# Kernel tuning notes

Hardware: AMD Instinct MI355X
Metric: run time of the kernel (lower is better)

The kernel has to match this reference:

```python
import jax, jax.numpy as jnp
import numpy as np

N_MODELS = 128
N_FEAT = 32
TREE_LAYERS = [64, 32, 16]
INPUT_SIZE = 512
BATCH = 8192
EPS = 1e-5


def _uniform(key, shape, fan_in, fan_out):
    stdv = np.sqrt(6.0 / (fan_in + fan_out))
    return jax.random.uniform(key, shape, jnp.float32, -stdv, stdv)


def setup_inputs() -> dict:
    key = jax.random.key(0)
    ks = jax.random.split(key, 8)
    x = jax.random.normal(ks[0], (BATCH, INPUT_SIZE), jnp.float32)
    # flattened per-tree feature indices, shape [n_models * n_feature]
    used_features = jax.random.randint(ks[1], (N_MODELS * N_FEAT,), 0, INPUT_SIZE, jnp.int32)
    W1 = _uniform(ks[2], (N_MODELS, N_FEAT, TREE_LAYERS[0]), N_FEAT, TREE_LAYERS[0])
    b1 = jnp.zeros((N_MODELS, 1, TREE_LAYERS[0]), jnp.float32)
    W2 = _uniform(ks[3], (N_MODELS, TREE_LAYERS[0], TREE_LAYERS[1]), TREE_LAYERS[0], TREE_LAYERS[1])
    b2 = jnp.zeros((N_MODELS, 1, TREE_LAYERS[1]), jnp.float32)
    W3 = _uniform(ks[4], (N_MODELS, TREE_LAYERS[1], TREE_LAYERS[2]), TREE_LAYERS[1], TREE_LAYERS[2])
    b3 = jnp.zeros((N_MODELS, 1, TREE_LAYERS[2]), jnp.float32)
    gamma1 = jnp.ones((N_MODELS * TREE_LAYERS[0],), jnp.float32)
    beta1 = jnp.zeros((N_MODELS * TREE_LAYERS[0],), jnp.float32)
    gamma2 = jnp.ones((N_MODELS * TREE_LAYERS[1],), jnp.float32)
    beta2 = jnp.zeros((N_MODELS * TREE_LAYERS[1],), jnp.float32)
    out_weight = jax.random.normal(ks[5], (N_MODELS * TREE_LAYERS[2], 1), jnp.float32)
    out_bias = jnp.zeros((1,), jnp.float32)
    return {
        "x": x, "used_features": used_features,
        "W1": W1, "b1": b1, "W2": W2, "b2": b2, "W3": W3, "b3": b3,
        "gamma1": gamma1, "beta1": beta1, "gamma2": gamma2, "beta2": beta2,
        "out_weight": out_weight, "out_bias": out_bias,
    }


def _batch_dense(h, W, b):
    # h: [B, n_models, in], W: [n_models, in, out], b: [n_models, 1, out]
    return jnp.einsum("bmi,mio->bmo", h, W) + b[None, :, 0, :]


def _batchnorm_train(z, gamma, beta):
    # BatchNorm1d in training mode over 2D input: per-feature batch stats (biased var)
    mean = jnp.mean(z, axis=0)
    var = jnp.var(z, axis=0)
    return (z - mean) * jax.lax.rsqrt(var + EPS) * gamma + beta


def reference(x, used_features, W1, b1, W2, b2, W3, b3,
              gamma1, beta1, gamma2, beta2, out_weight, out_bias):
    B = x.shape[0]
    # gather used features: [B, n_models * n_feature] -> [B, n_models, n_feature]
    h = x[:, used_features].reshape(B, N_MODELS, N_FEAT)
    # layer 1: grouped GEMM + BN + ReLU
    h = _batch_dense(h, W1, b1).reshape(B, -1)
    h = jax.nn.relu(_batchnorm_train(h, gamma1, beta1))
    # layer 2
    h = _batch_dense(h.reshape(B, N_MODELS, -1), W2, b2).reshape(B, -1)
    h = jax.nn.relu(_batchnorm_train(h, gamma2, beta2))
    # last layer (no BN/ReLU) -> pred
    pred = _batch_dense(h.reshape(B, N_MODELS, -1), W3, b3).reshape(B, -1)
    out = pred @ out_weight + out_bias
    return (out, pred)
```

## Files before the change

kernel.cpp:

```cpp
#include <hip/hip_runtime.h>
#include <hip/hip_bf16.h>

#define BATCH   8192
#define NM      128
#define NF      32
#define L1      64
#define L2O     32
#define L3O     16
#define INSZ    512
#define EPSV    1e-5f
#define CH      16
#define P64     64
#define GS1B    256
#define XS_STR  522
#define H1STR   80
#define H2STR   40

typedef __attribute__((ext_vector_type(8))) short short8;
typedef __attribute__((ext_vector_type(4))) float f32x4;

union U8 { short8 s8; unsigned u[4]; };

__device__ inline unsigned short f2bf(float f) {
    union { float f; unsigned u; } v; v.f = f;
    return (unsigned short)((v.u + 0x7FFF + ((v.u >> 16) & 1)) >> 16);
}
__device__ inline unsigned pkbf(float a, float b) {
    union { __hip_bfloat162 h; unsigned u; } c;
    c.h = __float22bfloat162_rn(float2{a, b});
    return c.u;
}

__global__ __launch_bounds__(256) void k_prep(
    const float* __restrict__ W1, const float* __restrict__ W2,
    const float* __restrict__ W3,
    unsigned short* __restrict__ W1p, unsigned short* __restrict__ W2p,
    unsigned short* __restrict__ W3p)
{
    int g = blockIdx.x*256 + threadIdx.x;
    int m = g / 4608, r = g % 4608;
    if (r < 2048) {
        int n = r >> 9, l = (r >> 3) & 63, s = r & 7;
        W1p[m*2048 + r] = f2bf(W1[m*2048 + ((l>>4)*8+s)*L1 + n*16 + (l&15)]);
    } else if (r < 4096) {
        int q = r - 2048;
        int f = q >> 9, l = (q >> 3) & 63, s = q & 7;
        int n2 = f >> 1, ks = f & 1;
        W2p[m*2048 + q] = f2bf(W2[m*2048 + (ks*32+(l>>4)*8+s)*L2O + n2*16 + (l&15)]);
    } else {
        int q = r - 4096;
        int l = (q >> 3) & 63, s = q & 7;
        W3p[m*512 + q] = f2bf(W3[m*512 + ((l>>4)*8+s)*L3O + (l&15)]);
    }
}

__global__ __launch_bounds__(512) void k_gs1(
    const float* __restrict__ x, const int* __restrict__ uf,
    const unsigned short* __restrict__ W1p,
    unsigned short* __restrict__ Ag,
    float* __restrict__ s1sum, float* __restrict__ s1sq)
{
    __shared__ unsigned short xs[32*XS_STR];
    __shared__ int sUf[NM*NF];
    const int blk = blockIdx.x, t = threadIdx.x;
    #pragma unroll
    for (int p = 0; p < 8; ++p) {
        const float4 v = *(const float4*)(x + (size_t)blk*32*INSZ + p*2048 + t*4);
        const int row = 4*p + (t>>7), col = (t&127)*4;
        *(unsigned*)(&xs[row*XS_STR + col])     = pkbf(v.x, v.y);
        *(unsigned*)(&xs[row*XS_STR + col + 2]) = pkbf(v.z, v.w);
    }
    #pragma unroll
    for (int p = 0; p < 2; ++p)
        ((int4*)sUf)[t + p*512] = ((const int4*)uf)[t + p*512];
    __syncthreads();

    const int w = t >> 6, l = t & 63, lr = l & 15, lg = l >> 4;
    const unsigned short* xr0 = xs + lr*XS_STR;
    const unsigned short* xr1 = xs + (16+lr)*XS_STR;
    for (int mi = 0; mi < 16; ++mi) {
        const int m = w*16 + mi;
        const int4 ia = ((const int4*)sUf)[m*8 + lg*2];
        const int4 ib = ((const int4*)sUf)[m*8 + lg*2 + 1];
        U8 A0, A1;
        A0.u[0] = xr0[ia.x] | ((unsigned)xr0[ia.y] << 16);
        A0.u[1] = xr0[ia.z] | ((unsigned)xr0[ia.w] << 16);
        A0.u[2] = xr0[ib.x] | ((unsigned)xr0[ib.y] << 16);
        A0.u[3] = xr0[ib.z] | ((unsigned)xr0[ib.w] << 16);
        A1.u[0] = xr1[ia.x] | ((unsigned)xr1[ia.y] << 16);
        A1.u[1] = xr1[ia.z] | ((unsigned)xr1[ia.w] << 16);
        A1.u[2] = xr1[ib.x] | ((unsigned)xr1[ib.y] << 16);
        A1.u[3] = xr1[ib.z] | ((unsigned)xr1[ib.w] << 16);
        *(short8*)(Ag + ((size_t)(blk*2  )*NM + m)*512 + lr*32 + lg*8) = A0.s8;
        *(short8*)(Ag + ((size_t)(blk*2+1)*NM + m)*512 + lr*32 + lg*8) = A1.s8;
        float sum[4], sq[4];
        #pragma unroll
        for (int n = 0; n < 4; ++n) {
            const short8 wf = *(const short8*)(W1p + m*2048 + n*512 + l*8);
            f32x4 z = {0.f,0.f,0.f,0.f};
            f32x4 c0 = __builtin_amdgcn_mfma_f32_16x16x32_bf16(A0.s8, wf, z, 0, 0, 0);
            f32x4 c1 = __builtin_amdgcn_mfma_f32_16x16x32_bf16(A1.s8, wf, z, 0, 0, 0);
            sum[n] = (c0[0]+c0[1]) + (c0[2]+c0[3]) + (c1[0]+c1[1]) + (c1[2]+c1[3]);
            sq[n]  = c0[0]*c0[0] + c0[1]*c0[1] + c0[2]*c0[2] + c0[3]*c0[3]
                   + c1[0]*c1[0] + c1[1]*c1[1] + c1[2]*c1[2] + c1[3]*c1[3];
        }
        #pragma unroll
        for (int n = 0; n < 4; ++n) {
            sum[n] += __shfl_xor(sum[n], 16); sum[n] += __shfl_xor(sum[n], 32);
            sq[n]  += __shfl_xor(sq[n], 16);  sq[n]  += __shfl_xor(sq[n], 32);
        }
        if (l < 16) {
            #pragma unroll
            for (int n = 0; n < 4; ++n) {
                s1sum[(size_t)blk*8192 + m*64 + n*16 + l] = sum[n];
                s1sq [(size_t)blk*8192 + m*64 + n*16 + l] = sq[n];
            }
        }
    }
}

__global__ __launch_bounds__(256) void k_fin(
    const float* __restrict__ sump, const float* __restrict__ sqp,
    const float* __restrict__ bias, const float* __restrict__ gamma,
    const float* __restrict__ beta, float* __restrict__ scale,
    float* __restrict__ shift, int nfeat, int parts, int slotMajor)
{
    int f = blockIdx.x*256 + threadIdx.x;
    if (f >= nfeat) return;
    float S = 0.f, Q = 0.f;
    if (slotMajor) {
        #pragma unroll 8
        for (int c = 0; c < parts; ++c) { S += sump[(size_t)c*nfeat + f]; Q += sqp[(size_t)c*nfeat + f]; }
    } else {
        #pragma unroll 8
        for (int c = 0; c < parts; ++c) { S += sump[(size_t)f*parts + c]; Q += sqp[(size_t)f*parts + c]; }
    }
    float mz   = S * (1.f/BATCH);
    float var  = Q * (1.f/BATCH) - mz*mz;
    float mean = mz + bias[f];
    float sc   = rsqrtf(var + EPSV) * gamma[f];
    scale[f] = sc; shift[f] = beta[f] - mean*sc;
}

__global__ __launch_bounds__(256) void k_stats2_p(
    const unsigned short* __restrict__ Ag, const unsigned short* __restrict__ W1p,
    const float* __restrict__ scale1, const float* __restrict__ shift1,
    const unsigned short* __restrict__ W2p,
    float* __restrict__ sum2p, float* __restrict__ sq2p)
{
    __shared__ unsigned short h1T[4][16*H1STR];
    const int m = blockIdx.x >> 4, chunk = blockIdx.x & 15;
    const int t = threadIdx.x, w = t >> 6, l = t & 63;
    const int lr = l & 15, lg = l >> 4;
    short8 w1f[4];
    #pragma unroll
    for (int n = 0; n < 4; ++n) w1f[n] = *(const short8*)(W1p + m*2048 + n*512 + l*8);
    short8 w2f[2][2];
    #pragma unroll
    for (int n2 = 0; n2 < 2; ++n2)
        #pragma unroll
        for (int ks = 0; ks < 2; ++ks)
            w2f[n2][ks] = *(const short8*)(W2p + m*2048 + (n2*2+ks)*512 + l*8);
    float4 sc1q[4], sh1q[4];
    #pragma unroll
    for (int n = 0; n < 4; ++n) {
        sc1q[n] = *(const float4*)(scale1 + m*L1 + n*16 + lg*4);
        sh1q[n] = *(const float4*)(shift1 + m*L1 + n*16 + lg*4);
    }
    unsigned short* hT = &h1T[w][0];
    float sumf[8] = {0,0,0,0,0,0,0,0}, sqf[8] = {0,0,0,0,0,0,0,0};
    for (int i = 0; i < 8; ++i) {
        const int rbG = chunk*32 + i*4 + w;
        const short8 a = *(const short8*)(Ag + ((size_t)rbG*NM + m)*512 + lr*32 + lg*8);
        #pragma unroll
        for (int n = 0; n < 4; ++n) {
            f32x4 z = {0.f,0.f,0.f,0.f};
            f32x4 acc = __builtin_amdgcn_mfma_f32_16x16x32_bf16(w1f[n], a, z, 0, 0, 0);
            float h0 = acc[0]*sc1q[n].x + sh1q[n].x; h0 = h0 > 0.f ? h0 : 0.f;
            float h1 = acc[1]*sc1q[n].y + sh1q[n].y; h1 = h1 > 0.f ? h1 : 0.f;
            float h2 = acc[2]*sc1q[n].z + sh1q[n].z; h2 = h2 > 0.f ? h2 : 0.f;
            float h3 = acc[3]*sc1q[n].w + sh1q[n].w; h3 = h3 > 0.f ? h3 : 0.f;
            uint2 pk; pk.x = pkbf(h0, h1); pk.y = pkbf(h2, h3);
            *(uint2*)(hT + lr*H1STR + n*16 + lg*4) = pk;
        }
        const short8 a20 = *(const short8*)(hT + lr*H1STR + lg*8);
        const short8 a21 = *(const short8*)(hT + lr*H1STR + 32 + lg*8);
        #pragma unroll
        for (int n2 = 0; n2 < 2; ++n2) {
            f32x4 z = {0.f,0.f,0.f,0.f};
            f32x4 acc = __builtin_amdgcn_mfma_f32_16x16x32_bf16(w2f[n2][0], a20, z, 0, 0, 0);
            acc = __builtin_amdgcn_mfma_f32_16x16x32_bf16(w2f[n2][1], a21, acc, 0, 0, 0);
            #pragma unroll
            for (int r = 0; r < 4; ++r) {
                sumf[n2*4+r] += acc[r];
                sqf [n2*4+r] += acc[r]*acc[r];
            }
        }
    }
    #pragma unroll
    for (int j = 0; j < 8; ++j) {
        #pragma unroll
        for (int mk = 1; mk < 16; mk <<= 1) {
            sumf[j] += __shfl_xor(sumf[j], mk);
            sqf[j]  += __shfl_xor(sqf[j], mk);
        }
    }
    if (lr == 0) {
        const int slot = chunk*4 + w;
        #pragma unroll
        for (int n2 = 0; n2 < 2; ++n2)
            #pragma unroll
            for (int r = 0; r < 4; ++r) {
                const int f = m*L2O + n2*16 + lg*4 + r;
                sum2p[(size_t)f*P64 + slot] = sumf[n2*4+r];
                sq2p [(size_t)f*P64 + slot] = sqf[n2*4+r];
            }
    }
}

__global__ __launch_bounds__(256) void k_final_p(
    const unsigned short* __restrict__ Ag, const unsigned short* __restrict__ W1p,
    const float* __restrict__ scale1, const float* __restrict__ shift1,
    const unsigned short* __restrict__ W2p,
    const float* __restrict__ scale2, const float* __restrict__ shift2,
    const unsigned short* __restrict__ W3p, const float* __restrict__ b3,
    const float* __restrict__ ow,
    float* __restrict__ pred, float* __restrict__ outpartT)
{
    __shared__ unsigned short h1T[4][16*H1STR];
    __shared__ unsigned short h2T[4][16*H2STR];
    const int m = blockIdx.x >> 4, chunk = blockIdx.x & 15;
    const int t = threadIdx.x, w = t >> 6, l = t & 63;
    const int lr = l & 15, lg = l >> 4;
    short8 w1f[4];
    #pragma unroll
    for (int n = 0; n < 4; ++n) w1f[n] = *(const short8*)(W1p + m*2048 + n*512 + l*8);
    short8 w2f[2][2];
    #pragma unroll
    for (int n2 = 0; n2 < 2; ++n2)
        #pragma unroll
        for (int ks = 0; ks < 2; ++ks)
            w2f[n2][ks] = *(const short8*)(W2p + m*2048 + (n2*2+ks)*512 + l*8);
    const short8 w3f = *(const short8*)(W3p + m*512 + l*8);
    float4 sc1q[4], sh1q[4];
    #pragma unroll
    for (int n = 0; n < 4; ++n) {
        sc1q[n] = *(const float4*)(scale1 + m*L1 + n*16 + lg*4);
        sh1q[n] = *(const float4*)(shift1 + m*L1 + n*16 + lg*4);
    }
    float4 sc2q[2], sh2q[2];
    #pragma unroll
    for (int n2 = 0; n2 < 2; ++n2) {
        sc2q[n2] = *(const float4*)(scale2 + m*L2O + n2*16 + lg*4);
        sh2q[n2] = *(const float4*)(shift2 + m*L2O + n2*16 + lg*4);
    }
    const float4 b3f = *(const float4*)(b3 + m*L3O + lg*4);
    const float4 owf = *(const float4*)(ow + m*L3O + lg*4);
    unsigned short* hT  = &h1T[w][0];
    unsigned short* hT2 = &h2T[w][0];
    for (int i = 0; i < 8; ++i) {
        const int rbG = chunk*32 + i*4 + w;
        const short8 a = *(const short8*)(Ag + ((size_t)rbG*NM + m)*512 + lr*32 + lg*8);
        #pragma unroll
        for (int n = 0; n < 4; ++n) {
            f32x4 z = {0.f,0.f,0.f,0.f};
            f32x4 acc = __builtin_amdgcn_mfma_f32_16x16x32_bf16(w1f[n], a, z, 0, 0, 0);
            float h0 = acc[0]*sc1q[n].x + sh1q[n].x; h0 = h0 > 0.f ? h0 : 0.f;
            float h1 = acc[1]*sc1q[n].y + sh1q[n].y; h1 = h1 > 0.f ? h1 : 0.f;
            float h2 = acc[2]*sc1q[n].z + sh1q[n].z; h2 = h2 > 0.f ? h2 : 0.f;
            float h3 = acc[3]*sc1q[n].w + sh1q[n].w; h3 = h3 > 0.f ? h3 : 0.f;
            uint2 pk; pk.x = pkbf(h0, h1); pk.y = pkbf(h2, h3);
            *(uint2*)(hT + lr*H1STR + n*16 + lg*4) = pk;
        }
        const short8 a20 = *(const short8*)(hT + lr*H1STR + lg*8);
        const short8 a21 = *(const short8*)(hT + lr*H1STR + 32 + lg*8);
        #pragma unroll
        for (int n2 = 0; n2 < 2; ++n2) {
            f32x4 z = {0.f,0.f,0.f,0.f};
            f32x4 acc = __builtin_amdgcn_mfma_f32_16x16x32_bf16(w2f[n2][0], a20, z, 0, 0, 0);
            acc = __builtin_amdgcn_mfma_f32_16x16x32_bf16(w2f[n2][1], a21, acc, 0, 0, 0);
            float h0 = acc[0]*sc2q[n2].x + sh2q[n2].x; h0 = h0 > 0.f ? h0 : 0.f;
            float h1 = acc[1]*sc2q[n2].y + sh2q[n2].y; h1 = h1 > 0.f ? h1 : 0.f;
            float h2 = acc[2]*sc2q[n2].z + sh2q[n2].z; h2 = h2 > 0.f ? h2 : 0.f;
            float h3 = acc[3]*sc2q[n2].w + sh2q[n2].w; h3 = h3 > 0.f ? h3 : 0.f;
            uint2 pk; pk.x = pkbf(h0, h1); pk.y = pkbf(h2, h3);
            *(uint2*)(hT2 + lr*H2STR + n2*16 + lg*4) = pk;
        }
        {
            const short8 a3 = *(const short8*)(hT2 + lr*H2STR + lg*8);
            f32x4 z = {0.f,0.f,0.f,0.f};
            f32x4 acc = __builtin_amdgcn_mfma_f32_16x16x32_bf16(w3f, a3, z, 0, 0, 0);
            float4 pv;
            pv.x = acc[0] + b3f.x; pv.y = acc[1] + b3f.y;
            pv.z = acc[2] + b3f.z; pv.w = acc[3] + b3f.w;
            const size_t row = (size_t)rbG*16 + lr;
            *(float4*)(pred + row*(NM*L3O) + m*L3O + lg*4) = pv;
            float v = pv.x*owf.x + pv.y*owf.y + pv.z*owf.z + pv.w*owf.w;
            v += __shfl_xor(v, 16); v += __shfl_xor(v, 32);
            if (l < 16) outpartT[(size_t)m*BATCH + rbG*16 + l] = v;
        }
    }
}

__global__ __launch_bounds__(256) void k_outT(
    const float* __restrict__ outpartT, const float* __restrict__ ob,
    float* __restrict__ out)
{
    int b = blockIdx.x*256 + threadIdx.x;
    float acc = ob[0];
    #pragma unroll 8
    for (int m = 0; m < NM; ++m) acc += outpartT[(size_t)m*BATCH + b];
    out[b] = acc;
}

__global__ __launch_bounds__(256) void k_gather(
    const float* __restrict__ x, const int* __restrict__ uf,
    unsigned short* __restrict__ Ag)
{
    __shared__ float xs[16*INSZ];
    __shared__ int   sUf[NM*NF];
    const int rb = blockIdx.x;
    const int t  = threadIdx.x;
    const float4* xsrc = (const float4*)(x + (size_t)rb*16*INSZ);
    float4* xdst = (float4*)xs;
    #pragma unroll
    for (int p = 0; p < 8; ++p) xdst[t + p*256] = xsrc[t + p*256];
    const int4* us = (const int4*)uf;
    int4* ud = (int4*)sUf;
    #pragma unroll
    for (int p = 0; p < 4; ++p) ud[t + p*256] = us[t + p*256];
    __syncthreads();
    unsigned* outp = (unsigned*)(Ag + (size_t)rb*NM*512);
    const int e = t*2, r = e >> 5, j = e & 31;
    for (int m = 0; m < NM; ++m) {
        const int i0 = sUf[m*NF + j], i1 = sUf[m*NF + j + 1];
        outp[m*256 + t] = pkbf(xs[r*INSZ + i0], xs[r*INSZ + i1]);
    }
}

__global__ __launch_bounds__(256) void k_stats1_m(
    const unsigned short* __restrict__ Ag, const unsigned short* __restrict__ W1p,
    float* __restrict__ sum1p, float* __restrict__ sq1p)
{
    const int m = blockIdx.x >> 4, chunk = blockIdx.x & 15;
    const int t = threadIdx.x, w = t >> 6, l = t & 63;
    const int lr = l & 15, lg = l >> 4;
    short8 w1f[4];
    #pragma unroll
    for (int n = 0; n < 4; ++n) w1f[n] = *(const short8*)(W1p + m*2048 + n*512 + l*8);
    float sum[4] = {0,0,0,0}, sq[4] = {0,0,0,0};
    for (int i = 0; i < 8; ++i) {
        const int rbG = chunk*32 + i*4 + w;
        const short8 a = *(const short8*)(Ag + ((size_t)rbG*NM + m)*512 + lr*32 + lg*8);
        #pragma unroll
        for (int n = 0; n < 4; ++n) {
            f32x4 acc = {0.f,0.f,0.f,0.f};
            acc = __builtin_amdgcn_mfma_f32_16x16x32_bf16(a, w1f[n], acc, 0, 0, 0);
            sum[n] += (acc[0]+acc[1]) + (acc[2]+acc[3]);
            sq[n]  += acc[0]*acc[0] + acc[1]*acc[1] + acc[2]*acc[2] + acc[3]*acc[3];
        }
    }
    #pragma unroll
    for (int n = 0; n < 4; ++n) {
        sum[n] += __shfl_xor(sum[n], 16); sum[n] += __shfl_xor(sum[n], 32);
        sq[n]  += __shfl_xor(sq[n], 16);  sq[n]  += __shfl_xor(sq[n], 32);
    }
    if (l < 16) {
        const int slot = chunk*4 + w;
        #pragma unroll
        for (int n = 0; n < 4; ++n) {
            const int f = m*L1 + n*16 + l;
            sum1p[(size_t)f*P64 + slot] = sum[n];
            sq1p [(size_t)f*P64 + slot] = sq[n];
        }
    }
}

extern "C" void kernel_launch(void* const* d_in, const int* in_sizes, int n_in,
                              void* d_out, int out_size, void* d_ws, size_t ws_size,
                              hipStream_t stream) {
    const float* x   = (const float*)d_in[0];
    const int*   uf  = (const int*  )d_in[1];
    const float* W1  = (const float*)d_in[2];
    const float* b1  = (const float*)d_in[3];
    const float* W2  = (const float*)d_in[4];
    const float* b2  = (const float*)d_in[5];
    const float* W3  = (const float*)d_in[6];
    const float* b3  = (const float*)d_in[7];
    const float* g1  = (const float*)d_in[8];
    const float* be1 = (const float*)d_in[9];
    const float* g2  = (const float*)d_in[10];
    const float* be2 = (const float*)d_in[11];
    const float* ow  = (const float*)d_in[12];
    const float* ob  = (const float*)d_in[13];

    float* out  = (float*)d_out;
    float* pred = out + BATCH;

    const size_t agElems = (size_t)BATCH * NM * NF;
    unsigned short* Ag  = (unsigned short*)d_ws;
    unsigned short* W1p = Ag + agElems;
    unsigned short* W2p = W1p + NM*2048;
    unsigned short* W3p = W2p + NM*2048;
    float* scale1 = (float*)(W3p + NM*512);
    float* shift1 = scale1 + NM*L1;
    float* scale2 = shift1 + NM*L1;
    float* shift2 = scale2 + NM*L2O;
    float* arena  = shift2 + NM*L2O;
    const size_t prefixBytes = (char*)arena - (char*)d_ws;

    const size_t arenaA = (size_t)GS1B*8192*4*2;
    const size_t s2Bytes = (size_t)NM*L2O*P64*4*2;
    const size_t needA = prefixBytes + arenaA;
    const size_t arenaB = (size_t)NM*L1*P64*4*2;
    (void)s2Bytes;

    k_prep<<<NM*4608/256, 256, 0, stream>>>(W1, W2, W3, W1p, W2p, W3p);

    if (ws_size >= needA) {
        float* s1sum = arena;
        float* s1sq  = s1sum + (size_t)GS1B*8192;
        float* s2sum = arena;
        float* s2sq  = s2sum + (size_t)NM*L2O*P64;
        float* outpartT = arena;

        k_gs1<<<GS1B, 512, 0, stream>>>(x, uf, W1p, Ag, s1sum, s1sq);
        k_fin<<<NM*L1/256, 256, 0, stream>>>(s1sum, s1sq, b1, g1, be1, scale1, shift1, NM*L1, GS1B, 1);
        k_stats2_p<<<NM*CH, 256, 0, stream>>>(Ag, W1p, scale1, shift1, W2p, s2sum, s2sq);
        k_fin<<<NM*L2O/256, 256, 0, stream>>>(s2sum, s2sq, b2, g2, be2, scale2, shift2, NM*L2O, P64, 0);
        k_final_p<<<NM*CH, 256, 0, stream>>>(Ag, W1p, scale1, shift1, W2p, scale2, shift2,
                                             W3p, b3, ow, pred, outpartT);
        k_outT<<<BATCH/256, 256, 0, stream>>>(outpartT, ob, out);
    } else {
        float* s1sum = arena;
        float* s1sq  = s1sum + (size_t)NM*L1*P64;
        float* outpartT = arena;
        float* s2sum = arena + arenaB/4;
        float* s2sq  = s2sum + (size_t)NM*L2O*P64;

        k_gather<<<BATCH/16, 256, 0, stream>>>(x, uf, Ag);
        k_stats1_m<<<NM*CH, 256, 0, stream>>>(Ag, W1p, s1sum, s1sq);
        k_fin<<<NM*L1/256, 256, 0, stream>>>(s1sum, s1sq, b1, g1, be1, scale1, shift1, NM*L1, P64, 0);
        k_stats2_p<<<NM*CH, 256, 0, stream>>>(Ag, W1p, scale1, shift1, W2p, s2sum, s2sq);
        k_fin<<<NM*L2O/256, 256, 0, stream>>>(s2sum, s2sq, b2, g2, be2, scale2, shift2, NM*L2O, P64, 0);
        k_final_p<<<NM*CH, 256, 0, stream>>>(Ag, W1p, scale1, shift1, W2p, scale2, shift2,
                                             W3p, b3, ow, pred, outpartT);
        k_outT<<<BATCH/256, 256, 0, stream>>>(outpartT, ob, out);
    }
}
```

Before: 115.4 us.

## Fuse whole MLP pipeline into one cooperative persistent kernel with grid syncs

Replaces the chain of gather, stats, finalize and output kernels with a single cooperative kernel of 256 blocks. Each block keeps its 32 input rows in LDS and regathers features for every phase, separated by grid-wide syncs for the BatchNorm statistics. This removes the global gathered-activation buffer, the per-tree output partials and the extra reduction kernel, so there are fewer launches and less memory traffic. In exchange each block recomputes layer 1 three times and layer 2 twice, with only 256 blocks of 8 waves resident. It needs cooperative launch support and falls back to the multi-kernel path when that launch fails.

```diff
diff --git a/kernel.cpp b/kernel.cpp
--- a/kernel.cpp
+++ b/kernel.cpp
@@ -1,5 +1,8 @@
 #include <hip/hip_runtime.h>
 #include <hip/hip_bf16.h>
+#include <hip/hip_cooperative_groups.h>
+
+namespace cg = cooperative_groups;
 
 #define BATCH   8192
 #define NM      128
@@ -54,6 +57,295 @@
     }
 }
 
+__device__ __forceinline__ void gatherAB(
+    const unsigned short* xr0, const unsigned short* xr1,
+    const int* sUf, int m, int lg, U8& A0, U8& A1)
+{
+    const int4 ia = ((const int4*)sUf)[m*8 + lg*2];
+    const int4 ib = ((const int4*)sUf)[m*8 + lg*2 + 1];
+    A0.u[0] = xr0[ia.x] | ((unsigned)xr0[ia.y] << 16);
+    A0.u[1] = xr0[ia.z] | ((unsigned)xr0[ia.w] << 16);
+    A0.u[2] = xr0[ib.x] | ((unsigned)xr0[ib.y] << 16);
+    A0.u[3] = xr0[ib.z] | ((unsigned)xr0[ib.w] << 16);
+    A1.u[0] = xr1[ia.x] | ((unsigned)xr1[ia.y] << 16);
+    A1.u[1] = xr1[ia.z] | ((unsigned)xr1[ia.w] << 16);
+    A1.u[2] = xr1[ib.x] | ((unsigned)xr1[ib.y] << 16);
+    A1.u[3] = xr1[ib.z] | ((unsigned)xr1[ib.w] << 16);
+}
+
+__device__ __forceinline__ void d1_tile(
+    const short8 a, const short8* w1f,
+    const float4* sc1q, const float4* sh1q,
+    unsigned short* hT, int lr, int lg)
+{
+    #pragma unroll
+    for (int n = 0; n < 4; ++n) {
+        f32x4 z = {0.f,0.f,0.f,0.f};
+        f32x4 acc = __builtin_amdgcn_mfma_f32_16x16x32_bf16(w1f[n], a, z, 0, 0, 0);
+        float h0 = acc[0]*sc1q[n].x + sh1q[n].x; h0 = h0 > 0.f ? h0 : 0.f;
+        float h1 = acc[1]*sc1q[n].y + sh1q[n].y; h1 = h1 > 0.f ? h1 : 0.f;
+        float h2 = acc[2]*sc1q[n].z + sh1q[n].z; h2 = h2 > 0.f ? h2 : 0.f;
+        float h3 = acc[3]*sc1q[n].w + sh1q[n].w; h3 = h3 > 0.f ? h3 : 0.f;
+        uint2 pk; pk.x = pkbf(h0, h1); pk.y = pkbf(h2, h3);
+        *(uint2*)(hT + lr*H1STR + n*16 + lg*4) = pk;
+    }
+}
+
+__device__ __forceinline__ float fin_tile_v(
+    const unsigned short* hT, unsigned short* hT2,
+    const short8 (*w2f)[2], const short8 w3f,
+    const float4* sc2q, const float4* sh2q,
+    const float4 b3f, const float4 owf,
+    int lr, int lg, int m, int rbG, float* __restrict__ pred)
+{
+    const short8 a20 = *(const short8*)(hT + lr*H1STR + lg*8);
+    const short8 a21 = *(const short8*)(hT + lr*H1STR + 32 + lg*8);
+    #pragma unroll
+    for (int n2 = 0; n2 < 2; ++n2) {
+        f32x4 z = {0.f,0.f,0.f,0.f};
+        f32x4 acc = __builtin_amdgcn_mfma_f32_16x16x32_bf16(w2f[n2][0], a20, z, 0, 0, 0);
+        acc = __builtin_amdgcn_mfma_f32_16x16x32_bf16(w2f[n2][1], a21, acc, 0, 0, 0);
+        float h0 = acc[0]*sc2q[n2].x + sh2q[n2].x; h0 = h0 > 0.f ? h0 : 0.f;
+        float h1 = acc[1]*sc2q[n2].y + sh2q[n2].y; h1 = h1 > 0.f ? h1 : 0.f;
+        float h2 = acc[2]*sc2q[n2].z + sh2q[n2].z; h2 = h2 > 0.f ? h2 : 0.f;
+        float h3 = acc[3]*sc2q[n2].w + sh2q[n2].w; h3 = h3 > 0.f ? h3 : 0.f;
+        uint2 pk; pk.x = pkbf(h0, h1); pk.y = pkbf(h2, h3);
+        *(uint2*)(hT2 + lr*H2STR + n2*16 + lg*4) = pk;
+    }
+    const short8 a3 = *(const short8*)(hT2 + lr*H2STR + lg*8);
+    f32x4 z = {0.f,0.f,0.f,0.f};
+    f32x4 acc = __builtin_amdgcn_mfma_f32_16x16x32_bf16(w3f, a3, z, 0, 0, 0);
+    float4 pv;
+    pv.x = acc[0] + b3f.x; pv.y = acc[1] + b3f.y;
+    pv.z = acc[2] + b3f.z; pv.w = acc[3] + b3f.w;
+    const size_t row = (size_t)rbG*16 + lr;
+    *(float4*)(pred + row*(NM*L3O) + m*L3O + lg*4) = pv;
+    float v = pv.x*owf.x + pv.y*owf.y + pv.z*owf.z + pv.w*owf.w;
+    v += __shfl_xor(v, 16); v += __shfl_xor(v, 32);
+    return v;
+}
+
+struct MegaArgs {
+    const float* x; const int* uf;
+    const unsigned short *W1p, *W2p, *W3p;
+    const float *b1, *g1, *be1, *b2, *g2, *be2, *b3, *ow, *ob;
+    float *scale1, *shift1, *scale2, *shift2;
+    float *s1sum, *s1sq, *s2sum, *s2sq;
+    float *pred, *out;
+};
+
+__global__ __launch_bounds__(512, 2) void k_mega(MegaArgs A)
+{
+    cg::grid_group gg = cg::this_grid();
+    __shared__ unsigned short xs[32*XS_STR];
+    __shared__ int sUf[NM*NF];
+    __shared__ unsigned short h1A[8][16*H1STR];
+    __shared__ unsigned short h1B[8][16*H1STR];
+    __shared__ unsigned short h2A[8][16*H2STR];
+    __shared__ unsigned short h2B[8][16*H2STR];
+    __shared__ float outLds[8][32];
+
+    const int blk = blockIdx.x, t = threadIdx.x;
+    #pragma unroll
+    for (int p = 0; p < 8; ++p) {
+        const float4 v = *(const float4*)(A.x + (size_t)blk*32*INSZ + p*2048 + t*4);
+        const int row = 4*p + (t>>7), col = (t&127)*4;
+        *(unsigned*)(&xs[row*XS_STR + col])     = pkbf(v.x, v.y);
+        *(unsigned*)(&xs[row*XS_STR + col + 2]) = pkbf(v.z, v.w);
+    }
+    #pragma unroll
+    for (int p = 0; p < 2; ++p)
+        ((int4*)sUf)[t + p*512] = ((const int4*)A.uf)[t + p*512];
+    __syncthreads();
+
+    const int w = t >> 6, l = t & 63, lr = l & 15, lg = l >> 4;
+    const unsigned short* xr0 = xs + lr*XS_STR;
+    const unsigned short* xr1 = xs + (16+lr)*XS_STR;
+
+    for (int mi = 0; mi < 16; ++mi) {
+        const int m = w*16 + mi;
+        U8 A0, A1;
+        gatherAB(xr0, xr1, sUf, m, lg, A0, A1);
+        float sum[4], sq[4];
+        #pragma unroll
+        for (int n = 0; n < 4; ++n) {
+            const short8 wf = *(const short8*)(A.W1p + m*2048 + n*512 + l*8);
+            f32x4 z = {0.f,0.f,0.f,0.f};
+            f32x4 c0 = __builtin_amdgcn_mfma_f32_16x16x32_bf16(A0.s8, wf, z, 0, 0, 0);
+            f32x4 c1 = __builtin_amdgcn_mfma_f32_16x16x32_bf16(A1.s8, wf, z, 0, 0, 0);
+            sum[n] = (c0[0]+c0[1]) + (c0[2]+c0[3]) + (c1[0]+c1[1]) + (c1[2]+c1[3]);
+            sq[n]  = c0[0]*c0[0] + c0[1]*c0[1] + c0[2]*c0[2] + c0[3]*c0[3]
+                   + c1[0]*c1[0] + c1[1]*c1[1] + c1[2]*c1[2] + c1[3]*c1[3];
+        }
+        #pragma unroll
+        for (int n = 0; n < 4; ++n) {
+            sum[n] += __shfl_xor(sum[n], 16); sum[n] += __shfl_xor(sum[n], 32);
+            sq[n]  += __shfl_xor(sq[n], 16);  sq[n]  += __shfl_xor(sq[n], 32);
+        }
+        if (l < 16) {
+            #pragma unroll
+            for (int n = 0; n < 4; ++n) {
+                A.s1sum[(size_t)blk*8192 + m*64 + n*16 + l] = sum[n];
+                A.s1sq [(size_t)blk*8192 + m*64 + n*16 + l] = sq[n];
+            }
+        }
+    }
+    __threadfence();
+    gg.sync();
+
+    {
+        const int fl = t >> 4, slice = t & 15;
+        const int f = blk*32 + fl;
+        float S = 0.f, Q = 0.f;
+        #pragma unroll 4
+        for (int k = 0; k < 16; ++k) {
+            const int c = slice + k*16;
+            S += A.s1sum[(size_t)c*8192 + f];
+            Q += A.s1sq [(size_t)c*8192 + f];
+        }
+        #pragma unroll
+        for (int mk = 1; mk < 16; mk <<= 1) { S += __shfl_xor(S, mk); Q += __shfl_xor(Q, mk); }
+        if (slice == 0) {
+            float mz   = S * (1.f/BATCH);
+            float var  = Q * (1.f/BATCH) - mz*mz;
+            float mean = mz + A.b1[f];
+            float sc   = rsqrtf(var + EPSV) * A.g1[f];
+            A.scale1[f] = sc; A.shift1[f] = A.be1[f] - mean*sc;
+        }
+    }
+    __threadfence();
+    gg.sync();
+
+    for (int mi = 0; mi < 16; ++mi) {
+        const int m = w*16 + mi;
+        U8 A0, A1;
+        gatherAB(xr0, xr1, sUf, m, lg, A0, A1);
+        short8 w1f[4];
+        #pragma unroll
+        for (int n = 0; n < 4; ++n) w1f[n] = *(const short8*)(A.W1p + m*2048 + n*512 + l*8);
+        float4 sc1q[4], sh1q[4];
+        #pragma unroll
+        for (int n = 0; n < 4; ++n) {
+            sc1q[n] = *(const float4*)(A.scale1 + m*L1 + n*16 + lg*4);
+            sh1q[n] = *(const float4*)(A.shift1 + m*L1 + n*16 + lg*4);
+        }
+        unsigned short* hTa = &h1A[w][0];
+        unsigned short* hTb = &h1B[w][0];
+        d1_tile(A0.s8, w1f, sc1q, sh1q, hTa, lr, lg);
+        d1_tile(A1.s8, w1f, sc1q, sh1q, hTb, lr, lg);
+        short8 w2f[2][2];
+        #pragma unroll
+        for (int n2 = 0; n2 < 2; ++n2)
+            #pragma unroll
+            for (int ks = 0; ks < 2; ++ks)
+                w2f[n2][ks] = *(const short8*)(A.W2p + m*2048 + (n2*2+ks)*512 + l*8);
+        float sumf[8] = {0,0,0,0,0,0,0,0}, sqf[8] = {0,0,0,0,0,0,0,0};
+        #pragma unroll
+        for (int half = 0; half < 2; ++half) {
+            const unsigned short* hT = half ? hTb : hTa;
+            const short8 a20 = *(const short8*)(hT + lr*H1STR + lg*8);
+            const short8 a21 = *(const short8*)(hT + lr*H1STR + 32 + lg*8);
+            #pragma unroll
+            for (int n2 = 0; n2 < 2; ++n2) {
+                f32x4 z = {0.f,0.f,0.f,0.f};
+                f32x4 acc = __builtin_amdgcn_mfma_f32_16x16x32_bf16(w2f[n2][0], a20, z, 0, 0, 0);
+                acc = __builtin_amdgcn_mfma_f32_16x16x32_bf16(w2f[n2][1], a21, acc, 0, 0, 0);
+                #pragma unroll
+                for (int r = 0; r < 4; ++r) { sumf[n2*4+r] += acc[r]; sqf[n2*4+r] += acc[r]*acc[r]; }
+            }
+        }
+        #pragma unroll
+        for (int j = 0; j < 8; ++j) {
+            #pragma unroll
+            for (int mk = 1; mk < 16; mk <<= 1) {
+                sumf[j] += __shfl_xor(sumf[j], mk);
+                sqf[j]  += __shfl_xor(sqf[j], mk);
+            }
+        }
+        if (lr == 0) {
+            #pragma unroll
+            for (int n2 = 0; n2 < 2; ++n2)
+                #pragma unroll
+                for (int r = 0; r < 4; ++r) {
+                    const int f = m*L2O + n2*16 + lg*4 + r;
+                    A.s2sum[(size_t)blk*4096 + f] = sumf[n2*4+r];
+                    A.s2sq [(size_t)blk*4096 + f] = sqf[n2*4+r];
+                }
+        }
+    }
+    __threadfence();
+    gg.sync();
+
+    {
+        const int fl = t >> 5, slice = t & 31;
+        const int f = blk*16 + fl;
+        float S = 0.f, Q = 0.f;
+        #pragma unroll
+        for (int k = 0; k < 8; ++k) {
+            const int c = slice + k*32;
+            S += A.s2sum[(size_t)c*4096 + f];
+            Q += A.s2sq [(size_t)c*4096 + f];
+        }
+        #pragma unroll
+        for (int mk = 1; mk < 32; mk <<= 1) { S += __shfl_xor(S, mk); Q += __shfl_xor(Q, mk); }
+        if (slice == 0) {
+            float mz   = S * (1.f/BATCH);
+            float var  = Q * (1.f/BATCH) - mz*mz;
+            float mean = mz + A.b2[f];
+            float sc   = rsqrtf(var + EPSV) * A.g2[f];
+            A.scale2[f] = sc; A.shift2[f] = A.be2[f] - mean*sc;
+        }
+    }
+    __threadfence();
+    gg.sync();
+
+    float vacc0 = 0.f, vacc1 = 0.f;
+    const int rbG0 = blk*2, rbG1 = blk*2 + 1;
+    for (int mi = 0; mi < 16; ++mi) {
+        const int m = w*16 + mi;
+        U8 A0, A1;
+        gatherAB(xr0, xr1, sUf, m, lg, A0, A1);
+        short8 w1f[4];
+        #pragma unroll
+        for (int n = 0; n < 4; ++n) w1f[n] = *(const short8*)(A.W1p + m*2048 + n*512 + l*8);
+        float4 sc1q[4], sh1q[4];
+        #pragma unroll
+        for (int n = 0; n < 4; ++n) {
+            sc1q[n] = *(const float4*)(A.scale1 + m*L1 + n*16 + lg*4);
+            sh1q[n] = *(const float4*)(A.shift1 + m*L1 + n*16 + lg*4);
+        }
+        unsigned short* hTa = &h1A[w][0];
+        unsigned short* hTb = &h1B[w][0];
+        d1_tile(A0.s8, w1f, sc1q, sh1q, hTa, lr, lg);
+        d1_tile(A1.s8, w1f, sc1q, sh1q, hTb, lr, lg);
+        short8 w2f[2][2];
+        #pragma unroll
+        for (int n2 = 0; n2 < 2; ++n2)
+            #pragma unroll
+            for (int ks = 0; ks < 2; ++ks)
+                w2f[n2][ks] = *(const short8*)(A.W2p + m*2048 + (n2*2+ks)*512 + l*8);
+        float4 sc2q[2], sh2q[2];
+        #pragma unroll
+        for (int n2 = 0; n2 < 2; ++n2) {
+            sc2q[n2] = *(const float4*)(A.scale2 + m*L2O + n2*16 + lg*4);
+            sh2q[n2] = *(const float4*)(A.shift2 + m*L2O + n2*16 + lg*4);
+        }
+        const short8 w3f = *(const short8*)(A.W3p + m*512 + l*8);
+        const float4 b3f = *(const float4*)(A.b3 + m*L3O + lg*4);
+        const float4 owf = *(const float4*)(A.ow + m*L3O + lg*4);
+        vacc0 += fin_tile_v(hTa, &h2A[w][0], w2f, w3f, sc2q, sh2q, b3f, owf, lr, lg, m, rbG0, A.pred);
+        vacc1 += fin_tile_v(hTb, &h2B[w][0], w2f, w3f, sc2q, sh2q, b3f, owf, lr, lg, m, rbG1, A.pred);
+    }
+    if (l < 16) { outLds[w][lr] = vacc0; outLds[w][16 + lr] = vacc1; }
+    __syncthreads();
+    if (t < 32) {
+        float s = A.ob[0];
+        #pragma unroll
+        for (int w2 = 0; w2 < 8; ++w2) s += outLds[w2][t];
+        A.out[blk*32 + t] = s;
+    }
+}
+
 __global__ __launch_bounds__(512) void k_gs1(
     const float* __restrict__ x, const int* __restrict__ uf,
     const unsigned short* __restrict__ W1p,
@@ -74,23 +366,13 @@
     for (int p = 0; p < 2; ++p)
         ((int4*)sUf)[t + p*512] = ((const int4*)uf)[t + p*512];
     __syncthreads();
-
     const int w = t >> 6, l = t & 63, lr = l & 15, lg = l >> 4;
     const unsigned short* xr0 = xs + lr*XS_STR;
     const unsigned short* xr1 = xs + (16+lr)*XS_STR;
     for (int mi = 0; mi < 16; ++mi) {
         const int m = w*16 + mi;
-        const int4 ia = ((const int4*)sUf)[m*8 + lg*2];
-        const int4 ib = ((const int4*)sUf)[m*8 + lg*2 + 1];
         U8 A0, A1;
-        A0.u[0] = xr0[ia.x] | ((unsigned)xr0[ia.y] << 16);
-        A0.u[1] = xr0[ia.z] | ((unsigned)xr0[ia.w] << 16);
-        A0.u[2] = xr0[ib.x] | ((unsigned)xr0[ib.y] << 16);
-        A0.u[3] = xr0[ib.z] | ((unsigned)xr0[ib.w] << 16);
-        A1.u[0] = xr1[ia.x] | ((unsigned)xr1[ia.y] << 16);
-        A1.u[1] = xr1[ia.z] | ((unsigned)xr1[ia.w] << 16);
-        A1.u[2] = xr1[ib.x] | ((unsigned)xr1[ib.y] << 16);
-        A1.u[3] = xr1[ib.z] | ((unsigned)xr1[ib.w] << 16);
+        gatherAB(xr0, xr1, sUf, m, lg, A0, A1);
         *(short8*)(Ag + ((size_t)(blk*2  )*NM + m)*512 + lr*32 + lg*8) = A0.s8;
         *(short8*)(Ag + ((size_t)(blk*2+1)*NM + m)*512 + lr*32 + lg*8) = A1.s8;
         float sum[4], sq[4];
@@ -172,17 +454,7 @@
     for (int i = 0; i < 8; ++i) {
         const int rbG = chunk*32 + i*4 + w;
         const short8 a = *(const short8*)(Ag + ((size_t)rbG*NM + m)*512 + lr*32 + lg*8);
-        #pragma unroll
-        for (int n = 0; n < 4; ++n) {
-            f32x4 z = {0.f,0.f,0.f,0.f};
-            f32x4 acc = __builtin_amdgcn_mfma_f32_16x16x32_bf16(w1f[n], a, z, 0, 0, 0);
-            float h0 = acc[0]*sc1q[n].x + sh1q[n].x; h0 = h0 > 0.f ? h0 : 0.f;
-            float h1 = acc[1]*sc1q[n].y + sh1q[n].y; h1 = h1 > 0.f ? h1 : 0.f;
-            float h2 = acc[2]*sc1q[n].z + sh1q[n].z; h2 = h2 > 0.f ? h2 : 0.f;
-            float h3 = acc[3]*sc1q[n].w + sh1q[n].w; h3 = h3 > 0.f ? h3 : 0.f;
-            uint2 pk; pk.x = pkbf(h0, h1); pk.y = pkbf(h2, h3);
-            *(uint2*)(hT + lr*H1STR + n*16 + lg*4) = pk;
-        }
+        d1_tile(a, w1f, sc1q, sh1q, hT, lr, lg);
         const short8 a20 = *(const short8*)(hT + lr*H1STR + lg*8);
         const short8 a21 = *(const short8*)(hT + lr*H1STR + 32 + lg*8);
         #pragma unroll
@@ -191,10 +463,7 @@
             f32x4 acc = __builtin_amdgcn_mfma_f32_16x16x32_bf16(w2f[n2][0], a20, z, 0, 0, 0);
             acc = __builtin_amdgcn_mfma_f32_16x16x32_bf16(w2f[n2][1], a21, acc, 0, 0, 0);
             #pragma unroll
-            for (int r = 0; r < 4; ++r) {
-                sumf[n2*4+r] += acc[r];
-                sqf [n2*4+r] += acc[r]*acc[r];
-            }
+            for (int r = 0; r < 4; ++r) { sumf[n2*4+r] += acc[r]; sqf[n2*4+r] += acc[r]*acc[r]; }
         }
     }
     #pragma unroll
@@ -261,44 +530,9 @@
     for (int i = 0; i < 8; ++i) {
         const int rbG = chunk*32 + i*4 + w;
         const short8 a = *(const short8*)(Ag + ((size_t)rbG*NM + m)*512 + lr*32 + lg*8);
-        #pragma unroll
-        for (int n = 0; n < 4; ++n) {
-            f32x4 z = {0.f,0.f,0.f,0.f};
-            f32x4 acc = __builtin_amdgcn_mfma_f32_16x16x32_bf16(w1f[n], a, z, 0, 0, 0);
-            float h0 = acc[0]*sc1q[n].x + sh1q[n].x; h0 = h0 > 0.f ? h0 : 0.f;
-            float h1 = acc[1]*sc1q[n].y + sh1q[n].y; h1 = h1 > 0.f ? h1 : 0.f;
-            float h2 = acc[2]*sc1q[n].z + sh1q[n].z; h2 = h2 > 0.f ? h2 : 0.f;
-            float h3 = acc[3]*sc1q[n].w + sh1q[n].w; h3 = h3 > 0.f ? h3 : 0.f;
-            uint2 pk; pk.x = pkbf(h0, h1); pk.y = pkbf(h2, h3);
-            *(uint2*)(hT + lr*H1STR + n*16 + lg*4) = pk;
-        }
-        const short8 a20 = *(const short8*)(hT + lr*H1STR + lg*8);
-        const short8 a21 = *(const short8*)(hT + lr*H1STR + 32 + lg*8);
-        #pragma unroll
-        for (int n2 = 0; n2 < 2; ++n2) {
-            f32x4 z = {0.f,0.f,0.f,0.f};
-            f32x4 acc = __builtin_amdgcn_mfma_f32_16x16x32_bf16(w2f[n2][0], a20, z, 0, 0, 0);
-            acc = __builtin_amdgcn_mfma_f32_16x16x32_bf16(w2f[n2][1], a21, acc, 0, 0, 0);
-            float h0 = acc[0]*sc2q[n2].x + sh2q[n2].x; h0 = h0 > 0.f ? h0 : 0.f;
-            float h1 = acc[1]*sc2q[n2].y + sh2q[n2].y; h1 = h1 > 0.f ? h1 : 0.f;
-            float h2 = acc[2]*sc2q[n2].z + sh2q[n2].z; h2 = h2 > 0.f ? h2 : 0.f;
-            float h3 = acc[3]*sc2q[n2].w + sh2q[n2].w; h3 = h3 > 0.f ? h3 : 0.f;
-            uint2 pk; pk.x = pkbf(h0, h1); pk.y = pkbf(h2, h3);
-            *(uint2*)(hT2 + lr*H2STR + n2*16 + lg*4) = pk;
-        }
-        {
-            const short8 a3 = *(const short8*)(hT2 + lr*H2STR + lg*8);
-            f32x4 z = {0.f,0.f,0.f,0.f};
-            f32x4 acc = __builtin_amdgcn_mfma_f32_16x16x32_bf16(w3f, a3, z, 0, 0, 0);
-            float4 pv;
-            pv.x = acc[0] + b3f.x; pv.y = acc[1] + b3f.y;
-            pv.z = acc[2] + b3f.z; pv.w = acc[3] + b3f.w;
-            const size_t row = (size_t)rbG*16 + lr;
-            *(float4*)(pred + row*(NM*L3O) + m*L3O + lg*4) = pv;
-            float v = pv.x*owf.x + pv.y*owf.y + pv.z*owf.z + pv.w*owf.w;
-            v += __shfl_xor(v, 16); v += __shfl_xor(v, 32);
-            if (l < 16) outpartT[(size_t)m*BATCH + rbG*16 + l] = v;
-        }
+        d1_tile(a, w1f, sc1q, sh1q, hT, lr, lg);
+        float v = fin_tile_v(hT, hT2, w2f, w3f, sc2q, sh2q, b3f, owf, lr, lg, m, rbG, pred);
+        if (l < 16) outpartT[(size_t)m*BATCH + rbG*16 + l] = v;
     }
 }
 
@@ -311,69 +545,6 @@
     #pragma unroll 8
     for (int m = 0; m < NM; ++m) acc += outpartT[(size_t)m*BATCH + b];
     out[b] = acc;
-}
-
-__global__ __launch_bounds__(256) void k_gather(
-    const float* __restrict__ x, const int* __restrict__ uf,
-    unsigned short* __restrict__ Ag)
-{
-    __shared__ float xs[16*INSZ];
-    __shared__ int   sUf[NM*NF];
-    const int rb = blockIdx.x;
-    const int t  = threadIdx.x;
-    const float4* xsrc = (const float4*)(x + (size_t)rb*16*INSZ);
-    float4* xdst = (float4*)xs;
-    #pragma unroll
-    for (int p = 0; p < 8; ++p) xdst[t + p*256] = xsrc[t + p*256];
-    const int4* us = (const int4*)uf;
-    int4* ud = (int4*)sUf;
-    #pragma unroll
-    for (int p = 0; p < 4; ++p) ud[t + p*256] = us[t + p*256];
-    __syncthreads();
-    unsigned* outp = (unsigned*)(Ag + (size_t)rb*NM*512);
-    const int e = t*2, r = e >> 5, j = e & 31;
-    for (int m = 0; m < NM; ++m) {
-        const int i0 = sUf[m*NF + j], i1 = sUf[m*NF + j + 1];
-        outp[m*256 + t] = pkbf(xs[r*INSZ + i0], xs[r*INSZ + i1]);
-    }
-}
-
-__global__ __launch_bounds__(256) void k_stats1_m(
-    const unsigned short* __restrict__ Ag, const unsigned short* __restrict__ W1p,
-    float* __restrict__ sum1p, float* __restrict__ sq1p)
-{
-    const int m = blockIdx.x >> 4, chunk = blockIdx.x & 15;
-    const int t = threadIdx.x, w = t >> 6, l = t & 63;
-    const int lr = l & 15, lg = l >> 4;
-    short8 w1f[4];
-    #pragma unroll
-    for (int n = 0; n < 4; ++n) w1f[n] = *(const short8*)(W1p + m*2048 + n*512 + l*8);
-    float sum[4] = {0,0,0,0}, sq[4] = {0,0,0,0};
-    for (int i = 0; i < 8; ++i) {
-        const int rbG = chunk*32 + i*4 + w;
-        const short8 a = *(const short8*)(Ag + ((size_t)rbG*NM + m)*512 + lr*32 + lg*8);
-        #pragma unroll
-        for (int n = 0; n < 4; ++n) {
-            f32x4 acc = {0.f,0.f,0.f,0.f};
-            acc = __builtin_amdgcn_mfma_f32_16x16x32_bf16(a, w1f[n], acc, 0, 0, 0);
-            sum[n] += (acc[0]+acc[1]) + (acc[2]+acc[3]);
-            sq[n]  += acc[0]*acc[0] + acc[1]*acc[1] + acc[2]*acc[2] + acc[3]*acc[3];
-        }
-    }
-    #pragma unroll
-    for (int n = 0; n < 4; ++n) {
-        sum[n] += __shfl_xor(sum[n], 16); sum[n] += __shfl_xor(sum[n], 32);
-        sq[n]  += __shfl_xor(sq[n], 16);  sq[n]  += __shfl_xor(sq[n], 32);
-    }
-    if (l < 16) {
-        const int slot = chunk*4 + w;
-        #pragma unroll
-        for (int n = 0; n < 4; ++n) {
-            const int f = m*L1 + n*16 + l;
-            sum1p[(size_t)f*P64 + slot] = sum[n];
-            sq1p [(size_t)f*P64 + slot] = sq[n];
-        }
-    }
 }
 
 extern "C" void kernel_launch(void* const* d_in, const int* in_sizes, int n_in,
@@ -397,54 +568,58 @@
     float* out  = (float*)d_out;
     float* pred = out + BATCH;
 
-    const size_t agElems = (size_t)BATCH * NM * NF;
-    unsigned short* Ag  = (unsigned short*)d_ws;
-    unsigned short* W1p = Ag + agElems;
+    unsigned short* W1p = (unsigned short*)d_ws;
     unsigned short* W2p = W1p + NM*2048;
     unsigned short* W3p = W2p + NM*2048;
     float* scale1 = (float*)(W3p + NM*512);
     float* shift1 = scale1 + NM*L1;
     float* scale2 = shift1 + NM*L1;
     float* shift2 = scale2 + NM*L2O;
-    float* arena  = shift2 + NM*L2O;
-    const size_t prefixBytes = (char*)arena - (char*)d_ws;
-
-    const size_t arenaA = (size_t)GS1B*8192*4*2;
-    const size_t s2Bytes = (size_t)NM*L2O*P64*4*2;
-    const size_t needA = prefixBytes + arenaA;
-    const size_t arenaB = (size_t)NM*L1*P64*4*2;
-    (void)s2Bytes;
+    float* s1sum  = shift2 + NM*L2O;
+    float* s1sq   = s1sum + (size_t)GS1B*8192;
+    float* s2sum  = s1sq  + (size_t)GS1B*8192;
+    float* s2sq   = s2sum + (size_t)GS1B*4096;
+    float* after  = s2sq  + (size_t)GS1B*4096;
+    const size_t megaBytes = (char*)after - (char*)d_ws;
 
     k_prep<<<NM*4608/256, 256, 0, stream>>>(W1, W2, W3, W1p, W2p, W3p);
 
-    if (ws_size >= needA) {
-        float* s1sum = arena;
-        float* s1sq  = s1sum + (size_t)GS1B*8192;
-        float* s2sum = arena;
-        float* s2sq  = s2sum + (size_t)NM*L2O*P64;
-        float* outpartT = arena;
+    int dev = 0, coop = 0;
+    hipGetDevice(&dev);
+    hipDeviceGetAttribute(&coop, hipDeviceAttributeCooperativeLaunch, dev);
+
+    bool launched = false;
+    if (coop && ws_size >= megaBytes) {
+        MegaArgs margs;
+        margs.x = x; margs.uf = uf;
+        margs.W1p = W1p; margs.W2p = W2p; margs.W3p = W3p;
+        margs.b1 = b1; margs.g1 = g1; margs.be1 = be1;
+        margs.b2 = b2; margs.g2 = g2; margs.be2 = be2;
+        margs.b3 = b3; margs.ow = ow; margs.ob = ob;
+        margs.scale1 = scale1; margs.shift1 = shift1;
+        margs.scale2 = scale2; margs.shift2 = shift2;
+        margs.s1sum = s1sum; margs.s1sq = s1sq;
+        margs.s2sum = s2sum; margs.s2sq = s2sq;
+        margs.pred = pred; margs.out = out;
+        void* params[] = { &margs };
+        hipError_t e = hipLaunchCooperativeKernel((const void*)k_mega,
+                                                  dim3(GS1B), dim3(512), params, 0, stream);
+        launched = (e == hipSuccess);
+    }
+
+    if (!launched) {
+        unsigned short* Ag = (unsigned short*)after;
+        float* arena = (float*)(Ag + (size_t)BATCH*NM*NF);
+        float* f_s2sum = arena;
+        float* f_s2sq  = f_s2sum + (size_t)NM*L2O*P64;
+        float* outpartT = f_s2sq + (size_t)NM*L2O*P64;
 
         k_gs1<<<GS1B, 512, 0, stream>>>(x, uf, W1p, Ag, s1sum, s1sq);
         k_fin<<<NM*L1/256, 256, 0, stream>>>(s1sum, s1sq, b1, g1, be1, scale1, shift1, NM*L1, GS1B, 1);
-        k_stats2_p<<<NM*CH, 256, 0, stream>>>(Ag, W1p, scale1, shift1, W2p, s2sum, s2sq);
-        k_fin<<<NM*L2O/256, 256, 0, stream>>>(s2sum, s2sq, b2, g2, be2, scale2, shift2, NM*L2O, P64, 0);
+        k_stats2_p<<<NM*CH, 256, 0, stream>>>(Ag, W1p, scale1, shift1, W2p, f_s2sum, f_s2sq);
+        k_fin<<<NM*L2O/256, 256, 0, stream>>>(f_s2sum, f_s2sq, b2, g2, be2, scale2, shift2, NM*L2O, P64, 0);
         k_final_p<<<NM*CH, 256, 0, stream>>>(Ag, W1p, scale1, shift1, W2p, scale2, shift2,
                                              W3p, b3, ow, pred, outpartT);
         k_outT<<<BATCH/256, 256, 0, stream>>>(outpartT, ob, out);
-    } else {
-        float* s1sum = arena;
-        float* s1sq  = s1sum + (size_t)NM*L1*P64;
-        float* outpartT = arena;
-        float* s2sum = arena + arenaB/4;
-        float* s2sq  = s2sum + (size_t)NM*L2O*P64;
-
-        k_gather<<<BATCH/16, 256, 0, stream>>>(x, uf, Ag);
-        k_stats1_m<<<NM*CH, 256, 0, stream>>>(Ag, W1p, s1sum, s1sq);
-        k_fin<<<NM*L1/256, 256, 0, stream>>>(s1sum, s1sq, b1, g1, be1, scale1, shift1, NM*L1, P64, 0);
-        k_stats2_p<<<NM*CH, 256, 0, stream>>>(Ag, W1p, scale1, shift1, W2p, s2sum, s2sq);
-        k_fin<<<NM*L2O/256, 256, 0, stream>>>(s2sum, s2sq, b2, g2, be2, scale2, shift2, NM*L2O, P64, 0);
-        k_final_p<<<NM*CH, 256, 0, stream>>>(Ag, W1p, scale1, shift1, W2p, scale2, shift2,
-                                             W3p, b3, ow, pred, outpartT);
-        k_outT<<<BATCH/256, 256, 0, stream>>>(outpartT, ob, out);
-    }
-}
+    }
+}
```

Result: slower. 424.0 us (+267.3%).

## Halve rows per k_gs1 block, drop LDS index staging, fold b3 into MFMA

Applied to the files above, without the earlier changes.

The gather+stats1 kernel now uses 512 blocks of 16 rows each instead of 256 blocks of 32 rows. That halves shared memory per block, removes the used_features staging into LDS (indices are read from global/cache instead), and is meant to raise occupancy and grid coverage on the CUs. The price is twice as many per-block partial stat rows for k_fin to reduce and a larger workspace arena, which could push execution onto the fallback path if the workspace is too small. Separately, the final kernel passes the b3 bias as the MFMA accumulator input instead of adding it afterward.

```diff
diff --git a/kernel.cpp b/kernel.cpp
--- a/kernel.cpp
+++ b/kernel.cpp
@@ -11,7 +11,7 @@
 #define EPSV    1e-5f
 #define CH      16
 #define P64     64
-#define GS1B    256
+#define GS1B    512
 #define XS_STR  522
 #define H1STR   80
 #define H2STR   40
@@ -60,49 +60,37 @@
     unsigned short* __restrict__ Ag,
     float* __restrict__ s1sum, float* __restrict__ s1sq)
 {
-    __shared__ unsigned short xs[32*XS_STR];
-    __shared__ int sUf[NM*NF];
+    __shared__ unsigned short xs[16*XS_STR];
     const int blk = blockIdx.x, t = threadIdx.x;
     #pragma unroll
-    for (int p = 0; p < 8; ++p) {
-        const float4 v = *(const float4*)(x + (size_t)blk*32*INSZ + p*2048 + t*4);
+    for (int p = 0; p < 4; ++p) {
+        const float4 v = *(const float4*)(x + (size_t)blk*16*INSZ + p*2048 + t*4);
         const int row = 4*p + (t>>7), col = (t&127)*4;
         *(unsigned*)(&xs[row*XS_STR + col])     = pkbf(v.x, v.y);
         *(unsigned*)(&xs[row*XS_STR + col + 2]) = pkbf(v.z, v.w);
     }
-    #pragma unroll
-    for (int p = 0; p < 2; ++p)
-        ((int4*)sUf)[t + p*512] = ((const int4*)uf)[t + p*512];
     __syncthreads();
 
     const int w = t >> 6, l = t & 63, lr = l & 15, lg = l >> 4;
     const unsigned short* xr0 = xs + lr*XS_STR;
-    const unsigned short* xr1 = xs + (16+lr)*XS_STR;
     for (int mi = 0; mi < 16; ++mi) {
         const int m = w*16 + mi;
-        const int4 ia = ((const int4*)sUf)[m*8 + lg*2];
-        const int4 ib = ((const int4*)sUf)[m*8 + lg*2 + 1];
-        U8 A0, A1;
+        const int4 ia = ((const int4*)uf)[m*8 + lg*2];
+        const int4 ib = ((const int4*)uf)[m*8 + lg*2 + 1];
+        U8 A0;
         A0.u[0] = xr0[ia.x] | ((unsigned)xr0[ia.y] << 16);
         A0.u[1] = xr0[ia.z] | ((unsigned)xr0[ia.w] << 16);
         A0.u[2] = xr0[ib.x] | ((unsigned)xr0[ib.y] << 16);
         A0.u[3] = xr0[ib.z] | ((unsigned)xr0[ib.w] << 16);
-        A1.u[0] = xr1[ia.x] | ((unsigned)xr1[ia.y] << 16);
-        A1.u[1] = xr1[ia.z] | ((unsigned)xr1[ia.w] << 16);
-        A1.u[2] = xr1[ib.x] | ((unsigned)xr1[ib.y] << 16);
-        A1.u[3] = xr1[ib.z] | ((unsigned)xr1[ib.w] << 16);
-        *(short8*)(Ag + ((size_t)(blk*2  )*NM + m)*512 + lr*32 + lg*8) = A0.s8;
-        *(short8*)(Ag + ((size_t)(blk*2+1)*NM + m)*512 + lr*32 + lg*8) = A1.s8;
+        *(short8*)(Ag + ((size_t)blk*NM + m)*512 + lr*32 + lg*8) = A0.s8;
         float sum[4], sq[4];
         #pragma unroll
         for (int n = 0; n < 4; ++n) {
             const short8 wf = *(const short8*)(W1p + m*2048 + n*512 + l*8);
             f32x4 z = {0.f,0.f,0.f,0.f};
             f32x4 c0 = __builtin_amdgcn_mfma_f32_16x16x32_bf16(A0.s8, wf, z, 0, 0, 0);
-            f32x4 c1 = __builtin_amdgcn_mfma_f32_16x16x32_bf16(A1.s8, wf, z, 0, 0, 0);
-            sum[n] = (c0[0]+c0[1]) + (c0[2]+c0[3]) + (c1[0]+c1[1]) + (c1[2]+c1[3]);
-            sq[n]  = c0[0]*c0[0] + c0[1]*c0[1] + c0[2]*c0[2] + c0[3]*c0[3]
-                   + c1[0]*c1[0] + c1[1]*c1[1] + c1[2]*c1[2] + c1[3]*c1[3];
+            sum[n] = (c0[0]+c0[1]) + (c0[2]+c0[3]);
+            sq[n]  = c0[0]*c0[0] + c0[1]*c0[1] + c0[2]*c0[2] + c0[3]*c0[3];
         }
         #pragma unroll
         for (int n = 0; n < 4; ++n) {
@@ -256,6 +244,7 @@
     }
     const float4 b3f = *(const float4*)(b3 + m*L3O + lg*4);
     const float4 owf = *(const float4*)(ow + m*L3O + lg*4);
+    f32x4 cb3; cb3[0] = b3f.x; cb3[1] = b3f.y; cb3[2] = b3f.z; cb3[3] = b3f.w;
     unsigned short* hT  = &h1T[w][0];
     unsigned short* hT2 = &h2T[w][0];
     for (int i = 0; i < 8; ++i) {
@@ -288,11 +277,9 @@
         }
         {
             const short8 a3 = *(const short8*)(hT2 + lr*H2STR + lg*8);
-            f32x4 z = {0.f,0.f,0.f,0.f};
-            f32x4 acc = __builtin_amdgcn_mfma_f32_16x16x32_bf16(w3f, a3, z, 0, 0, 0);
+            f32x4 acc = __builtin_amdgcn_mfma_f32_16x16x32_bf16(w3f, a3, cb3, 0, 0, 0);
             float4 pv;
-            pv.x = acc[0] + b3f.x; pv.y = acc[1] + b3f.y;
-            pv.z = acc[2] + b3f.z; pv.w = acc[3] + b3f.w;
+            pv.x = acc[0]; pv.y = acc[1]; pv.z = acc[2]; pv.w = acc[3];
             const size_t row = (size_t)rbG*16 + lr;
             *(float4*)(pred + row*(NM*L3O) + m*L3O + lg*4) = pv;
             float v = pv.x*owf.x + pv.y*owf.y + pv.z*owf.z + pv.w*owf.w;
@@ -410,10 +397,8 @@
     const size_t prefixBytes = (char*)arena - (char*)d_ws;
 
     const size_t arenaA = (size_t)GS1B*8192*4*2;
-    const size_t s2Bytes = (size_t)NM*L2O*P64*4*2;
     const size_t needA = prefixBytes + arenaA;
     const size_t arenaB = (size_t)NM*L1*P64*4*2;
-    (void)s2Bytes;
 
     k_prep<<<NM*4608/256, 256, 0, stream>>>(W1, W2, W3, W1p, W2p, W3p);
 
```

New measurement: 132.8 us. 1.15x slower.
